# Performance work log

Hardware: AMD Instinct MI355X
Metric: run time of the kernel (lower is better)

## Reference

```python
import jax, jax.numpy as jnp
import numpy as np

N, E, G = 50000, 800000, 16
H, C = 4, 64  # heads, per-head channels
NEG_SLOPE = 0.2

def gat_conv(x, src, dst, W, att_s, att_d, bias, heads, out_c, concat):
    # x: [N, Fin]; W: [Fin, heads*out_c]; att_s/att_d: [heads, out_c]
    h = (x @ W).reshape(N, heads, out_c)
    a_s = (h * att_s).sum(-1)              # [N, heads]
    a_d = (h * att_d).sum(-1)
    e = a_s[src] + a_d[dst]                # [E, heads]
    e = jnp.where(e >= 0, e, NEG_SLOPE * e)  # leaky_relu
    m = jax.ops.segment_max(e, dst, num_segments=N)
    ex = jnp.exp(e - m[dst])
    den = jax.ops.segment_sum(ex, dst, num_segments=N)
    alpha = ex / (den[dst] + 1e-16)        # segment softmax over incoming edges
    msg = h[src] * alpha[:, :, None]       # [E, heads, out_c]
    out = jax.ops.segment_sum(msg, dst, num_segments=N)
    out = out.reshape(N, heads * out_c) if concat else out.mean(axis=1)
    return out + bias

def setup_inputs() -> dict:
    key = jax.random.key(0)
    ks = jax.random.split(key, 30)
    def g(k, shape, scale=0.05):
        return (jax.random.normal(k, shape, dtype=jnp.float32) * scale)
    inp = {}
    inp['x'] = jax.random.normal(ks[0], (N, 32), dtype=jnp.float32)
    inp['edge_index'] = jax.random.randint(ks[1], (2, E), 0, N, dtype=jnp.int32)
    inp['batch'] = jnp.sort(jax.random.randint(ks[2], (N,), 0, G, dtype=jnp.int32))
    inp['global_features'] = jax.random.normal(ks[3], (G, 4), dtype=jnp.float32)
    # node encoder
    inp['W_enc'] = g(ks[4], (32, C)); inp['b_enc'] = g(ks[5], (C,))
    # conv1: 64 -> 4x64 concat
    inp['W1'] = g(ks[6], (C, H * C)); inp['as1'] = g(ks[7], (H, C)); inp['ad1'] = g(ks[8], (H, C)); inp['b1'] = g(ks[9], (H * C,))
    # conv2: 256 -> 4x64 concat
    inp['W2'] = g(ks[10], (H * C, H * C)); inp['as2'] = g(ks[11], (H, C)); inp['ad2'] = g(ks[12], (H, C)); inp['b2'] = g(ks[13], (H * C,))
    # conv3: 256 -> 1x64 no concat
    inp['W3'] = g(ks[14], (H * C, C)); inp['as3'] = g(ks[15], (1, C)); inp['ad3'] = g(ks[16], (1, C)); inp['b3'] = g(ks[17], (C,))
    # global processor
    inp['Wg'] = g(ks[18], (4, C)); inp['bg'] = g(ks[19], (C,))
    # decoder
    inp['Wd1'] = g(ks[20], (2 * C, C)); inp['bd1'] = g(ks[21], (C,))
    inp['gamma'] = jnp.ones((C,), jnp.float32); inp['beta'] = jnp.zeros((C,), jnp.float32)
    inp['Wd2'] = g(ks[22], (C, 256)); inp['bd2'] = g(ks[23], (256,))
    return inp

def reference(x, edge_index, batch, global_features, W_enc, b_enc,
              W1, as1, ad1, b1, W2, as2, ad2, b2, W3, as3, ad3, b3,
              Wg, bg, Wd1, bd1, gamma, beta, Wd2, bd2):
    # add self-loops (PyG GATConv default)
    loops = jnp.arange(N, dtype=edge_index.dtype)
    src = jnp.concatenate([edge_index[0], loops])
    dst = jnp.concatenate([edge_index[1], loops])
    h = x @ W_enc + b_enc
    h = gat_conv(h, src, dst, W1, as1, ad1, b1, H, C, True)
    h = jax.nn.elu(h)  # dropout is identity in eval
    h = gat_conv(h, src, dst, W2, as2, ad2, b2, H, C, True)
    h = jax.nn.elu(h)
    h = gat_conv(h, src, dst, W3, as3, ad3, b3, 1, C, False)
    # global mean pool per graph
    sums = jax.ops.segment_sum(h, batch, num_segments=G)
    cnts = jax.ops.segment_sum(jnp.ones((N, 1), h.dtype), batch, num_segments=G)
    pooled = sums / jnp.maximum(cnts, 1.0)
    genc = jax.nn.relu(global_features @ Wg + bg)
    z = jnp.concatenate([pooled, genc], axis=1)
    z = z @ Wd1 + bd1
    z = z * gamma + beta  # BatchNorm1d in eval mode (running stats 0/1)
    z = jax.nn.relu(z)
    out = z @ Wd2 + bd2
    return jax.nn.softmax(out, axis=1)
```

## Files before the change

### kernel.cpp

```cpp
#include <hip/hip_runtime.h>
#include <math.h>

#define NEG_SLOPE 0.2f
#define LOG2E 1.4426950408889634f

typedef __attribute__((ext_vector_type(8))) short short8;
typedef __attribute__((ext_vector_type(4))) float f32x4;
typedef __attribute__((ext_vector_type(2))) float f32x2;

#if __has_builtin(__builtin_amdgcn_cvt_pk_f32_fp8) && __has_builtin(__builtin_amdgcn_cvt_pk_fp8_f32)
#define FP8_HW 1
#else
#define FP8_HW 0
#endif

__device__ inline float b2f_lo(unsigned int u) {
    union { unsigned int i; float f; } x; x.i = u << 16; return x.f;
}
__device__ inline float b2f_hi(unsigned int u) {
    union { unsigned int i; float f; } x; x.i = u & 0xFFFF0000u; return x.f;
}
__device__ inline unsigned short f2b(float f) {
    union { float f; unsigned int i; } u; u.f = f;
    unsigned int r = u.i + 0x7FFF + ((u.i >> 16) & 1);
    return (unsigned short)(r >> 16);
}

__device__ inline float fp8_decode1(unsigned int b) {
    unsigned int e = (b >> 3) & 15, m = b & 7;
    union { unsigned int i; float f; } u;
    if (e == 0) u.f = (float)m * 0.001953125f;
    else u.i = ((e + 120) << 23) | (m << 20);
    if (b & 0x80) u.f = -u.f;
    return u.f;
}
__device__ inline void fp8x4_to_f32(unsigned int g, float& v0, float& v1,
                                    float& v2, float& v3) {
#if FP8_HW
    f32x2 lo = __builtin_amdgcn_cvt_pk_f32_fp8((int)g, false);
    f32x2 hi = __builtin_amdgcn_cvt_pk_f32_fp8((int)g, true);
    v0 = lo[0]; v1 = lo[1]; v2 = hi[0]; v3 = hi[1];
#else
    v0 = fp8_decode1(g & 255);         v1 = fp8_decode1((g >> 8) & 255);
    v2 = fp8_decode1((g >> 16) & 255); v3 = fp8_decode1((g >> 24) & 255);
#endif
}
__device__ inline void fp8x2_to_f32(unsigned int g2, float& v0, float& v1) {
#if FP8_HW
    f32x2 lo = __builtin_amdgcn_cvt_pk_f32_fp8((int)(g2 & 0xFFFF), false);
    v0 = lo[0]; v1 = lo[1];
#else
    v0 = fp8_decode1(g2 & 255);
    v1 = fp8_decode1((g2 >> 8) & 255);
#endif
}
__device__ inline unsigned char f32_to_fp8(float f) {
#if FP8_HW
    return (unsigned char)(__builtin_amdgcn_cvt_pk_fp8_f32(f, f, 0, false) & 0xFF);
#else
    union { float f; unsigned int i; } u; u.f = f;
    unsigned int s = (u.i >> 24) & 0x80;
    float a = fabsf(f);
    if (a < 0.015625f) {
        int m = (int)rintf(a * 512.0f);
        if (m > 7) return (unsigned char)(s | 0x08);
        return (unsigned char)(s | m);
    }
    if (a >= 448.0f) return (unsigned char)(s | 0x7E);
    int e = (int)((u.i >> 23) & 0xFF) - 127;
    union { unsigned int i; float f; } sc; sc.i = (unsigned int)(127 + 3 - e) << 23;
    int q = (int)rintf(a * sc.f);
    if (q >= 16) { q = 8; e += 1; }
    return (unsigned char)(s | ((unsigned int)(e + 7) << 3) | (unsigned int)(q - 8));
#endif
}

__global__ void prep_kernel(const float* __restrict__ W_enc, const float* __restrict__ b_enc,
                            const float* __restrict__ W1, const float* __restrict__ W2,
                            const float* __restrict__ W3, const float* __restrict__ as1,
                            const float* __restrict__ ad1, const float* __restrict__ b1,
                            const float* __restrict__ as3, const float* __restrict__ ad3,
                            unsigned short* __restrict__ Wc1t, float* __restrict__ bc1,
                            unsigned short* __restrict__ Wt2, unsigned short* __restrict__ Wt3,
                            float* __restrict__ u1s, float* __restrict__ u1d,
                            float* __restrict__ u3s, float* __restrict__ u3d,
                            int* __restrict__ counts, float* __restrict__ pooledP,
                            float* __restrict__ cntP, int N, int G, int zc) {
    const int b = blockIdx.x;
    const int t = threadIdx.x;
    if (b < 32) {
        int i = b * 256 + t;
        int h = i >> 11, rem = i & 2047, o = rem >> 5, j = rem & 31;
        float s = 0.0f;
        for (int k = 0; k < 64; k++)
            s += W_enc[j * 64 + k] * W1[k * 256 + h * 64 + o];
        Wc1t[i] = f2b(s);
    } else if (b == 32) {
        float s = b1[t];
        for (int k = 0; k < 64; k++) s += b_enc[k] * W1[k * 256 + t];
        bc1[t] = s;
    } else if (b == 33) {
        int k = t >> 2, h = t & 3;
        float s = 0.0f, d = 0.0f;
        for (int c = 0; c < 64; c++) {
            float w = W1[k * 256 + h * 64 + c];
            s += w * as1[h * 64 + c];
            d += w * ad1[h * 64 + c];
        }
        u1s[k * 4 + h] = s;
        u1d[k * 4 + h] = d;
    } else if (b == 34) {
        float s = 0.0f, d = 0.0f;
        for (int o = 0; o < 64; o++) {
            float w = W3[t * 64 + o];
            s += w * as3[o];
            d += w * ad3[o];
        }
        u3s[t] = s; u3d[t] = d;
    } else if (b < 35 + 256) {
        int i = (b - 35) * 256 + t;
        int k = i >> 8, m = i & 255;
        Wt2[(size_t)m * 256 + k] = f2b(W2[i]);
    } else if (b < 35 + 256 + 64) {
        int i = (b - 291) * 256 + t;
        int k = i >> 6, m = i & 63;
        Wt3[(size_t)m * 256 + k] = f2b(W3[i]);
    } else if (b < 355 + zc) {
        int i = (b - 355) * 256 + t;
        if (i < N) counts[i] = 0;
    } else {
        int i = (b - 355 - zc) * 256 + t;
        if (i < 64 * G * 64) pooledP[i] = 0.0f;
        if (i < 64 * G) cntP[i] = 0.0f;
    }
}

__global__ __launch_bounds__(256) void score_x(
        const float* __restrict__ x, const float* __restrict__ W_enc,
        const float* __restrict__ b_enc,
        const float* __restrict__ u1s, const float* __restrict__ u1d,
        unsigned char* __restrict__ x8, float* __restrict__ a_s,
        float* __restrict__ a_d, int N) {
    __shared__ float sUs[32][4], sUd[32][4], sC[8];
    __shared__ float sX[32][33];
    const int t = threadIdx.x;
    if (t < 128) {
        int j = t >> 2, h = t & 3;
        float s = 0.0f, d = 0.0f;
        for (int k = 0; k < 64; k++) {
            float w = W_enc[j * 64 + k];
            s += w * u1s[k * 4 + h];
            d += w * u1d[k * 4 + h];
        }
        sUs[j][h] = s; sUd[j][h] = d;
    } else if (t < 136) {
        int hh = t - 128;
        const float* u = (hh < 4) ? u1s : u1d;
        int h = hh & 3;
        float c = 0.0f;
        for (int k = 0; k < 64; k++) c += b_enc[k] * u[k * 4 + h];
        sC[hh] = c;
    }
    const int n0 = blockIdx.x * 32;
    const int row = t >> 3, col = (t & 7) << 2;
    float4 xv = {0, 0, 0, 0};
    if (n0 + row < N) xv = *(const float4*)&x[(size_t)(n0 + row) * 32 + col];
    sX[row][col + 0] = xv.x; sX[row][col + 1] = xv.y;
    sX[row][col + 2] = xv.z; sX[row][col + 3] = xv.w;
    __syncthreads();
    const int ni = t >> 3, oi = t & 7, h = oi & 3;
    const bool isS = oi < 4;
    float acc = sC[oi];
    #pragma unroll 8
    for (int j = 0; j < 32; j++) acc += sX[ni][j] * (isS ? sUs[j][h] : sUd[j][h]);
    if (n0 + ni < N) {
        float* out = isS ? a_s : a_d;
        out[(size_t)(n0 + ni) * 4 + h] = acc * LOG2E;
    }
    if (n0 + row < N) {
        unsigned int o = (unsigned int)f32_to_fp8(xv.x)
                       | ((unsigned int)f32_to_fp8(xv.y) << 8)
                       | ((unsigned int)f32_to_fp8(xv.z) << 16)
                       | ((unsigned int)f32_to_fp8(xv.w) << 24);
        *(unsigned int*)&x8[(size_t)(n0 + row) * 32 + col] = o;
    }
}

__global__ __launch_bounds__(256) void gemm_c12(
        const unsigned short* __restrict__ aggX,
        const unsigned short* __restrict__ Wc1t,
        const float* __restrict__ bc1,
        const unsigned short* __restrict__ Wt2,
        const float* __restrict__ att_s,
        const float* __restrict__ att_d,
        float* __restrict__ a_s, float* __restrict__ a_d,
        unsigned char* __restrict__ C8,
        int Nrows) {
    __shared__ unsigned short sH[64][264];
    __shared__ unsigned short sB[256][40];
    __shared__ float sSD[64][4][2];
    const int tid = threadIdx.x;
    const int wave = tid >> 6;
    const int lane = tid & 63;
    const int quad = lane >> 4;
    const int l16 = lane & 15;
    const int row0 = blockIdx.x * 64;
    const int sr = tid >> 2;
    const int sk = (tid & 3) << 3;

    #pragma unroll
    for (int h = 0; h < 4; h++) {
        __syncthreads();
        {
            int r = row0 + sr;
            uint4 z = {0,0,0,0};
            *(uint4*)&sB[sr][sk] = (r < Nrows)
                ? *(const uint4*)&aggX[(size_t)r * 128 + h * 32 + sk] : z;
            *(uint4*)&sB[64 + sr][sk] = *(const uint4*)&Wc1t[(size_t)(h * 64 + sr) * 32 + sk];
        }
        __syncthreads();
        short8 bf = *(const short8*)&sB[64 + wave * 16 + l16][quad * 8];
        const int col = h * 64 + wave * 16 + l16;
        const float bb = bc1[col];
        #pragma unroll
        for (int i = 0; i < 4; i++) {
            short8 af = *(const short8*)&sB[i * 16 + l16][quad * 8];
            f32x4 acc = __builtin_amdgcn_mfma_f32_16x16x32_bf16(af, bf, (f32x4){0,0,0,0}, 0, 0, 0);
            #pragma unroll
            for (int r = 0; r < 4; r++) {
                float v = acc[r] + bb;
                v = (v > 0.0f) ? v : expm1f(v);
                sH[i * 16 + quad * 4 + r][col] = f2b(v);
            }
        }
    }

    f32x4 acc2[4][4];
    #pragma unroll
    for (int i = 0; i < 4; i++)
        #pragma unroll
        for (int j = 0; j < 4; j++) acc2[i][j] = (f32x4){0,0,0,0};

    for (int kt = 0; kt < 256; kt += 32) {
        __syncthreads();
        #pragma unroll
        for (int i = 0; i < 4; i++) {
            int c = sr + i * 64;
            *(uint4*)&sB[c][sk] = *(const uint4*)&Wt2[(size_t)c * 256 + kt + sk];
        }
        __syncthreads();
        short8 bf2[4];
        #pragma unroll
        for (int j = 0; j < 4; j++)
            bf2[j] = *(const short8*)&sB[wave * 64 + j * 16 + l16][quad * 8];
        #pragma unroll
        for (int i = 0; i < 4; i++) {
            short8 af = *(const short8*)&sH[i * 16 + l16][kt + quad * 8];
            #pragma unroll
            for (int j = 0; j < 4; j++)
                acc2[i][j] = __builtin_amdgcn_mfma_f32_16x16x32_bf16(af, bf2[j], acc2[i][j], 0, 0, 0);
        }
    }

    {
        for (int t = tid; t < 512; t += 256) ((float*)sSD)[t] = 0.0f;
        __syncthreads();
        float avs[4], avd[4];
        #pragma unroll
        for (int j = 0; j < 4; j++) {
            int c = wave * 64 + j * 16 + l16;
            avs[j] = att_s[c];
            avd[j] = att_d[c];
        }
        #pragma unroll
        for (int i = 0; i < 4; i++) {
            float ps[4] = {0,0,0,0}, pd[4] = {0,0,0,0};
            #pragma unroll
            for (int j = 0; j < 4; j++)
                #pragma unroll
                for (int r = 0; r < 4; r++) {
                    ps[r] += acc2[i][j][r] * avs[j];
                    pd[r] += acc2[i][j][r] * avd[j];
                }
            #pragma unroll
            for (int off = 1; off < 16; off <<= 1)
                #pragma unroll
                for (int r = 0; r < 4; r++) {
                    ps[r] += __shfl_xor(ps[r], off);
                    pd[r] += __shfl_xor(pd[r], off);
                }
            if (l16 == 0) {
                #pragma unroll
                for (int r = 0; r < 4; r++) {
                    atomicAdd(&sSD[i * 16 + quad * 4 + r][wave][0], ps[r]);
                    atomicAdd(&sSD[i * 16 + quad * 4 + r][wave][1], pd[r]);
                }
            }
        }
        __syncthreads();
        {
            int row = tid & 63, hb = tid >> 6;
            int r = row0 + row;
            if (r < Nrows) {
                a_s[r * 4 + hb] = sSD[row][hb][0] * LOG2E;
                a_d[r * 4 + hb] = sSD[row][hb][1] * LOG2E;
            }
        }
    }
    #pragma unroll
    for (int i = 0; i < 4; i++) {
        #pragma unroll
        for (int j = 0; j < 4; j++) {
            int col = wave * 64 + j * 16 + l16;
            #pragma unroll
            for (int r = 0; r < 4; r++) {
                int row = row0 + i * 16 + quad * 4 + r;
                if (row < Nrows) C8[(size_t)row * 256 + col] = f32_to_fp8(acc2[i][j][r]);
            }
        }
    }
}

__global__ __launch_bounds__(256) void gemm_c3(const unsigned short* __restrict__ A16,
                                               const unsigned short* __restrict__ Bt16,
                                               unsigned char* __restrict__ C8,
                                               int Nrows) {
    __shared__ unsigned short sA[64][40];
    __shared__ unsigned short sB[64][40];
    const int tid = threadIdx.x;
    const int wave = tid >> 6;
    const int lane = tid & 63;
    const int quad = lane >> 4;
    const int l16 = lane & 15;
    const int row0 = blockIdx.x * 64;
    const int sr = tid >> 2;
    const int sk = (tid & 3) << 3;

    f32x4 acc[4];
    #pragma unroll
    for (int i = 0; i < 4; i++) acc[i] = (f32x4){0,0,0,0};

    for (int kt = 0; kt < 256; kt += 32) {
        __syncthreads();
        {
            int r = row0 + sr;
            uint4 z = {0,0,0,0};
            *(uint4*)&sA[sr][sk] = (r < Nrows) ? *(const uint4*)&A16[(size_t)r * 256 + kt + sk] : z;
            *(uint4*)&sB[sr][sk] = *(const uint4*)&Bt16[(size_t)sr * 256 + kt + sk];
        }
        __syncthreads();
        short8 bf = *(const short8*)&sB[wave * 16 + l16][quad * 8];
        #pragma unroll
        for (int i = 0; i < 4; i++) {
            short8 af = *(const short8*)&sA[i * 16 + l16][quad * 8];
            acc[i] = __builtin_amdgcn_mfma_f32_16x16x32_bf16(af, bf, acc[i], 0, 0, 0);
        }
    }
    const int col = wave * 16 + l16;
    #pragma unroll
    for (int i = 0; i < 4; i++) {
        #pragma unroll
        for (int r = 0; r < 4; r++) {
            int row = row0 + i * 16 + quad * 4 + r;
            if (row < Nrows) C8[(size_t)row * 64 + col] = f32_to_fp8(acc[i][r]);
        }
    }
}

__global__ void edge_hist_kernel(const int* __restrict__ ei, int* __restrict__ counts,
                                 int E, int Et) {
    int e = blockIdx.x * 256 + threadIdx.x;
    if (e >= Et) return;
    int d = (e < E) ? ei[E + e] : e - E;
    atomicAdd(&counts[d], 1);
}

__global__ __launch_bounds__(1024) void scan_blocks(int* __restrict__ counts,
                                                    int* __restrict__ blockSums, int N) {
    __shared__ int wsum[16];
    const int tid = threadIdx.x;
    const int lane = tid & 63;
    const int wave = tid >> 6;
    int i = blockIdx.x * 1024 + tid;
    int v = (i < N) ? counts[i] : 0;
    int s = v;
    #pragma unroll
    for (int off = 1; off < 64; off <<= 1) {
        int t = __shfl_up(s, off);
        if (lane >= off) s += t;
    }
    if (lane == 63) wsum[wave] = s;
    __syncthreads();
    if (wave == 0 && lane < 16) {
        int ws = wsum[lane];
        #pragma unroll
        for (int off = 1; off < 16; off <<= 1) {
            int t = __shfl_up(ws, off);
            if (lane >= off) ws += t;
        }
        wsum[lane] = ws;
    }
    __syncthreads();
    int waveOff = (wave > 0) ? wsum[wave - 1] : 0;
    int incl = s + waveOff;
    if (i < N) counts[i] = incl - v;
    if (tid == 1023) blockSums[blockIdx.x] = incl;
}

__global__ void scan_add2(const int* __restrict__ excl, const int* __restrict__ blockSums,
                          int nb, int* __restrict__ offsets, int* __restrict__ cursor,
                          int N, int Et) {
    __shared__ int sbs[64];
    if (threadIdx.x < 64) {
        int lane = threadIdx.x;
        int v = (lane < nb) ? blockSums[lane] : 0;
        int s = v;
        #pragma unroll
        for (int off = 1; off < 64; off <<= 1) {
            int t = __shfl_up(s, off);
            if (lane >= off) s += t;
        }
        sbs[lane] = s - v;
    }
    __syncthreads();
    int i = blockIdx.x * 256 + threadIdx.x;
    if (i < N) {
        int o = excl[i] + sbs[i >> 10];
        offsets[i] = o;
        cursor[i] = o;
    }
    if (i == N) offsets[N] = Et;
}

__global__ void edge_sort_kernel(const int* __restrict__ ei, int* __restrict__ cursor,
                                 int* __restrict__ srcS, int E, int Et) {
    int e = blockIdx.x * 256 + threadIdx.x;
    if (e >= Et) return;
    int s, d;
    if (e < E) { s = ei[e]; d = ei[E + e]; } else { s = d = e - E; }
    int pos = atomicAdd(&cursor[d], 1);
    srcS[pos] = s;
}

__global__ __launch_bounds__(256) void gat_agg_x32(
        const int* __restrict__ offsets, const int* __restrict__ srcS,
        const float4* __restrict__ a_s4, const float4* __restrict__ a_d4,
        const unsigned char* __restrict__ x8,
        unsigned short* __restrict__ aggX,
        int N) {
    __shared__ float4 wlds[4][64];
    __shared__ int slds[4][64];
    const int wid = threadIdx.x >> 6;
    const int n = blockIdx.x * 4 + wid;
    if (n >= N) return;
    const int lane = threadIdx.x & 63;
    const int q = lane >> 4;
    const int l16 = lane & 15;
    const int start = offsets[n], end = offsets[n + 1];
    const float4 ad = a_d4[n];
    float2 acc0 = {0,0}, acc1 = {0,0}, acc2 = {0,0}, acc3 = {0,0};
    float4 den = {0,0,0,0};
    const int loff = l16 << 1;

    for (int e0 = start; e0 < end; e0 += 64) {
        const int cnt = min(64, end - e0);
        if (lane < cnt) {
            int sB = srcS[e0 + lane];
            slds[wid][lane] = sB;
            const float4 as = a_s4[sB];
            float x0 = as.x + ad.x; x0 = fmaxf(x0, NEG_SLOPE * x0);
            float x1 = as.y + ad.y; x1 = fmaxf(x1, NEG_SLOPE * x1);
            float x2 = as.z + ad.z; x2 = fmaxf(x2, NEG_SLOPE * x2);
            float x3 = as.w + ad.w; x3 = fmaxf(x3, NEG_SLOPE * x3);
            wlds[wid][lane] = (float4){exp2f(x0), exp2f(x1), exp2f(x2), exp2f(x3)};
        }
        int j = q;
        for (; j + 12 < cnt; j += 16) {
            int ss[4]; float4 ww[4]; unsigned int gg[4];
            #pragma unroll
            for (int u = 0; u < 4; u++) {
                ss[u] = slds[wid][j + 4 * u];
                ww[u] = wlds[wid][j + 4 * u];
            }
            #pragma unroll
            for (int u = 0; u < 4; u++)
                gg[u] = *(const unsigned short*)&x8[((size_t)ss[u] << 5) + loff];
            #pragma unroll
            for (int u = 0; u < 4; u++) {
                float vl, vh;
                fp8x2_to_f32(gg[u], vl, vh);
                acc0.x += ww[u].x * vl; acc0.y += ww[u].x * vh;
                acc1.x += ww[u].y * vl; acc1.y += ww[u].y * vh;
                acc2.x += ww[u].z * vl; acc2.y += ww[u].z * vh;
                acc3.x += ww[u].w * vl; acc3.y += ww[u].w * vh;
                den.x += ww[u].x; den.y += ww[u].y; den.z += ww[u].z; den.w += ww[u].w;
            }
        }
        for (; j + 4 < cnt; j += 8) {
            const int s0 = slds[wid][j], s1 = slds[wid][j + 4];
            const float4 w0 = wlds[wid][j], w1 = wlds[wid][j + 4];
            const unsigned int g0 = *(const unsigned short*)&x8[((size_t)s0 << 5) + loff];
            const unsigned int g1 = *(const unsigned short*)&x8[((size_t)s1 << 5) + loff];
            float vl0, vh0, vl1, vh1;
            fp8x2_to_f32(g0, vl0, vh0);
            fp8x2_to_f32(g1, vl1, vh1);
            acc0.x += w0.x * vl0 + w1.x * vl1; acc0.y += w0.x * vh0 + w1.x * vh1;
            acc1.x += w0.y * vl0 + w1.y * vl1; acc1.y += w0.y * vh0 + w1.y * vh1;
            acc2.x += w0.z * vl0 + w1.z * vl1; acc2.y += w0.z * vh0 + w1.z * vh1;
            acc3.x += w0.w * vl0 + w1.w * vl1; acc3.y += w0.w * vh0 + w1.w * vh1;
            den.x += w0.x + w1.x; den.y += w0.y + w1.y;
            den.z += w0.z + w1.z; den.w += w0.w + w1.w;
        }
        for (; j < cnt; j += 4) {
            const int s = slds[wid][j];
            const float4 w = wlds[wid][j];
            const unsigned int g = *(const unsigned short*)&x8[((size_t)s << 5) + loff];
            float vl, vh;
            fp8x2_to_f32(g, vl, vh);
            acc0.x += w.x * vl; acc0.y += w.x * vh;
            acc1.x += w.y * vl; acc1.y += w.y * vh;
            acc2.x += w.z * vl; acc2.y += w.z * vh;
            acc3.x += w.w * vl; acc3.y += w.w * vh;
            den.x += w.x; den.y += w.y; den.z += w.z; den.w += w.w;
        }
    }
    #pragma unroll
    for (int off = 16; off < 64; off <<= 1) {
        acc0.x += __shfl_xor(acc0.x, off); acc0.y += __shfl_xor(acc0.y, off);
        acc1.x += __shfl_xor(acc1.x, off); acc1.y += __shfl_xor(acc1.y, off);
        acc2.x += __shfl_xor(acc2.x, off); acc2.y += __shfl_xor(acc2.y, off);
        acc3.x += __shfl_xor(acc3.x, off); acc3.y += __shfl_xor(acc3.y, off);
        den.x += __shfl_xor(den.x, off); den.y += __shfl_xor(den.y, off);
        den.z += __shfl_xor(den.z, off); den.w += __shfl_xor(den.w, off);
    }
    if (q == 0) {
        const float i0 = 1.0f / (den.x + 1e-16f);
        const float i1 = 1.0f / (den.y + 1e-16f);
        const float i2 = 1.0f / (den.z + 1e-16f);
        const float i3 = 1.0f / (den.w + 1e-16f);
        unsigned int o0 = (unsigned int)f2b(acc0.x * i0) | ((unsigned int)f2b(acc0.y * i0) << 16);
        unsigned int o1 = (unsigned int)f2b(acc1.x * i1) | ((unsigned int)f2b(acc1.y * i1) << 16);
        unsigned int o2 = (unsigned int)f2b(acc2.x * i2) | ((unsigned int)f2b(acc2.y * i2) << 16);
        unsigned int o3 = (unsigned int)f2b(acc3.x * i3) | ((unsigned int)f2b(acc3.y * i3) << 16);
        *(unsigned int*)&aggX[((size_t)n << 7) + 0 * 32 + loff] = o0;
        *(unsigned int*)&aggX[((size_t)n << 7) + 1 * 32 + loff] = o1;
        *(unsigned int*)&aggX[((size_t)n << 7) + 2 * 32 + loff] = o2;
        *(unsigned int*)&aggX[((size_t)n << 7) + 3 * 32 + loff] = o3;
    }
}

__global__ __launch_bounds__(256) void gat_fused4(
        const int* __restrict__ offsets, const int* __restrict__ srcS,
        const float4* __restrict__ a_s4, const float4* __restrict__ a_d4,
        const unsigned char* __restrict__ h8, const float* __restrict__ bias,
        const float* __restrict__ u3s, const float* __restrict__ u3d,
        float* __restrict__ a_s3, float* __restrict__ a_d3,
        unsigned short* __restrict__ out16, int N) {
    __shared__ float wlds[4][64][4];
    __shared__ int slds[4][64];
    const int wid = threadIdx.x >> 6;
    const int n = blockIdx.x * 4 + wid;
    if (n >= N) return;
    const int lane = threadIdx.x & 63;
    const int quad = lane >> 4;
    const int start = offsets[n], end = offsets[n + 1];
    const float4 ad = a_d4[n];
    float4 acc = {0, 0, 0, 0};
    float den = 0.0f;
    const int loff = lane << 2;

    for (int e0 = start; e0 < end; e0 += 64) {
        const int cnt = min(64, end - e0);
        if (lane < cnt) {
            int sB = srcS[e0 + lane];
            slds[wid][lane] = sB;
            const float4 as = a_s4[sB];
            float x0 = as.x + ad.x; x0 = fmaxf(x0, NEG_SLOPE * x0);
            float x1 = as.y + ad.y; x1 = fmaxf(x1, NEG_SLOPE * x1);
            float x2 = as.z + ad.z; x2 = fmaxf(x2, NEG_SLOPE * x2);
            float x3 = as.w + ad.w; x3 = fmaxf(x3, NEG_SLOPE * x3);
            wlds[wid][lane][0] = exp2f(x0);
            wlds[wid][lane][1] = exp2f(x1);
            wlds[wid][lane][2] = exp2f(x2);
            wlds[wid][lane][3] = exp2f(x3);
        }
        int j = 0;
        for (; j + 4 <= cnt; j += 4) {
            const int s0 = __builtin_amdgcn_readfirstlane(slds[wid][j + 0]);
            const int s1 = __builtin_amdgcn_readfirstlane(slds[wid][j + 1]);
            const int s2 = __builtin_amdgcn_readfirstlane(slds[wid][j + 2]);
            const int s3 = __builtin_amdgcn_readfirstlane(slds[wid][j + 3]);
            const float w0 = wlds[wid][j + 0][quad];
            const float w1 = wlds[wid][j + 1][quad];
            const float w2 = wlds[wid][j + 2][quad];
            const float w3 = wlds[wid][j + 3][quad];
            const unsigned int g0 = *(const unsigned int*)&h8[((size_t)s0 << 8) + loff];
            const unsigned int g1 = *(const unsigned int*)&h8[((size_t)s1 << 8) + loff];
            const unsigned int g2 = *(const unsigned int*)&h8[((size_t)s2 << 8) + loff];
            const unsigned int g3 = *(const unsigned int*)&h8[((size_t)s3 << 8) + loff];
            float v0, v1, v2, v3;
            fp8x4_to_f32(g0, v0, v1, v2, v3);
            acc.x += w0 * v0; acc.y += w0 * v1; acc.z += w0 * v2; acc.w += w0 * v3;
            fp8x4_to_f32(g1, v0, v1, v2, v3);
            acc.x += w1 * v0; acc.y += w1 * v1; acc.z += w1 * v2; acc.w += w1 * v3;
            fp8x4_to_f32(g2, v0, v1, v2, v3);
            acc.x += w2 * v0; acc.y += w2 * v1; acc.z += w2 * v2; acc.w += w2 * v3;
            fp8x4_to_f32(g3, v0, v1, v2, v3);
            acc.x += w3 * v0; acc.y += w3 * v1; acc.z += w3 * v2; acc.w += w3 * v3;
            den += (w0 + w1) + (w2 + w3);
        }
        for (; j < cnt; j++) {
            const int s = __builtin_amdgcn_readfirstlane(slds[wid][j]);
            const float w = wlds[wid][j][quad];
            const unsigned int g = *(const unsigned int*)&h8[((size_t)s << 8) + loff];
            float v0, v1, v2, v3;
            fp8x4_to_f32(g, v0, v1, v2, v3);
            acc.x += w * v0; acc.y += w * v1; acc.z += w * v2; acc.w += w * v3;
            den += w;
        }
    }

    const float inv = 1.0f / (den + 1e-16f);
    const float4 bb = *(const float4*)&bias[loff];
    float v0 = acc.x * inv + bb.x; v0 = (v0 > 0.0f) ? v0 : expm1f(v0);
    float v1 = acc.y * inv + bb.y; v1 = (v1 > 0.0f) ? v1 : expm1f(v1);
    float v2 = acc.z * inv + bb.z; v2 = (v2 > 0.0f) ? v2 : expm1f(v2);
    float v3 = acc.w * inv + bb.w; v3 = (v3 > 0.0f) ? v3 : expm1f(v3);
    {
        const float4 us = *(const float4*)&u3s[loff];
        const float4 ud = *(const float4*)&u3d[loff];
        float ps = v0 * us.x + v1 * us.y + v2 * us.z + v3 * us.w;
        float pd = v0 * ud.x + v1 * ud.y + v2 * ud.z + v3 * ud.w;
        #pragma unroll
        for (int off = 1; off < 64; off <<= 1) {
            ps += __shfl_xor(ps, off);
            pd += __shfl_xor(pd, off);
        }
        if (lane == 0) {
            a_s3[n] = ps * LOG2E;
            a_d3[n] = pd * LOG2E;
        }
    }
    uint2 o;
    o.x = (unsigned int)f2b(v0) | ((unsigned int)f2b(v1) << 16);
    o.y = (unsigned int)f2b(v2) | ((unsigned int)f2b(v3) << 16);
    *(uint2*)&out16[(size_t)n * 256 + loff] = o;
}

__global__ __launch_bounds__(256) void gat_fused1(
        const int* __restrict__ offsets, const int* __restrict__ srcS,
        const float* __restrict__ a_s, const float* __restrict__ a_d,
        const unsigned char* __restrict__ h8, const float* __restrict__ bias,
        const int* __restrict__ batch,
        float* __restrict__ pooledP, float* __restrict__ cntP, int N, int G) {
    __shared__ float wlds[4][64];
    __shared__ int slds[4][64];
    __shared__ float2 sOut[4][32];
    __shared__ int sG[4];
    const int wid = threadIdx.x >> 6;
    const int n = blockIdx.x * 4 + wid;
    const bool valid = n < N;
    const int lane = threadIdx.x & 63;
    const int half = lane >> 5;
    const int l32 = lane & 31;
    const int start = valid ? offsets[n] : 0;
    const int end   = valid ? offsets[n + 1] : 0;
    const float ad  = valid ? a_d[n] : 0.0f;
    float accx = 0.0f, accy = 0.0f, den = 0.0f;
    const int loff = l32 << 1;

    for (int e0 = start; e0 < end; e0 += 64) {
        const int cnt_ = min(64, end - e0);
        if (lane < cnt_) {
            int sB = srcS[e0 + lane];
            slds[wid][lane] = sB;
            float ev = a_s[sB] + ad;
            ev = fmaxf(ev, NEG_SLOPE * ev);
            wlds[wid][lane] = exp2f(ev);
        }
        int j = half;
        for (; j + 8 <= cnt_ + half; j += 8) {
            const int s0 = slds[wid][j + 0];
            const int s1 = slds[wid][j + 2];
            const int s2 = slds[wid][j + 4];
            const int s3 = slds[wid][j + 6];
            const float w0 = wlds[wid][j + 0];
            const float w1 = wlds[wid][j + 2];
            const float w2 = wlds[wid][j + 4];
            const float w3 = wlds[wid][j + 6];
            const unsigned int g0 = *(const unsigned short*)&h8[((size_t)s0 << 6) + loff];
            const unsigned int g1 = *(const unsigned short*)&h8[((size_t)s1 << 6) + loff];
            const unsigned int g2 = *(const unsigned short*)&h8[((size_t)s2 << 6) + loff];
            const unsigned int g3 = *(const unsigned short*)&h8[((size_t)s3 << 6) + loff];
            float vl, vh;
            fp8x2_to_f32(g0, vl, vh); accx += w0 * vl; accy += w0 * vh;
            fp8x2_to_f32(g1, vl, vh); accx += w1 * vl; accy += w1 * vh;
            fp8x2_to_f32(g2, vl, vh); accx += w2 * vl; accy += w2 * vh;
            fp8x2_to_f32(g3, vl, vh); accx += w3 * vl; accy += w3 * vh;
            den += (w0 + w1) + (w2 + w3);
        }
        for (; j < cnt_; j += 2) {
            const int s = slds[wid][j];
            const float w = wlds[wid][j];
            const unsigned int g = *(const unsigned short*)&h8[((size_t)s << 6) + loff];
            float vl, vh;
            fp8x2_to_f32(g, vl, vh);
            accx += w * vl;
            accy += w * vh;
            den += w;
        }
    }
    accx += __shfl_xor(accx, 32);
    accy += __shfl_xor(accy, 32);
    den  += __shfl_xor(den, 32);
    if (half == 0) {
        if (valid) {
            const float inv = 1.0f / (den + 1e-16f);
            sOut[wid][l32] = (float2){accx * inv + bias[loff], accy * inv + bias[loff + 1]};
        } else {
            sOut[wid][l32] = (float2){0.0f, 0.0f};
        }
        if (l32 == 0) sG[wid] = valid ? batch[n] : -1;
    }
    __syncthreads();
    const int p = blockIdx.x & 63;
    if (wid == 0 && half == 0) {
        const int g0 = sG[0], g1 = sG[1], g2 = sG[2], g3 = sG[3];
        if (g0 >= 0 && g1 == g0 && g2 == g0 && g3 == g0) {
            const float2 s0 = sOut[0][l32], s1 = sOut[1][l32];
            const float2 s2 = sOut[2][l32], s3 = sOut[3][l32];
            float* base = pooledP + ((size_t)p * G + g0) * 64;
            atomicAdd(&base[loff],     (s0.x + s1.x) + (s2.x + s3.x));
            atomicAdd(&base[loff + 1], (s0.y + s1.y) + (s2.y + s3.y));
            if (l32 == 0) atomicAdd(&cntP[p * G + g0], 4.0f);
        } else {
            #pragma unroll
            for (int w = 0; w < 4; w++) {
                const int g = sG[w];
                if (g >= 0) {
                    const float2 s = sOut[w][l32];
                    float* base = pooledP + ((size_t)p * G + g) * 64;
                    atomicAdd(&base[loff], s.x);
                    atomicAdd(&base[loff + 1], s.y);
                    if (l32 == 0) atomicAdd(&cntP[p * G + g], 1.0f);
                }
            }
        }
    }
}

__global__ __launch_bounds__(256) void final_kernel(
        const float* __restrict__ pooledP, const float* __restrict__ cntP,
        const float* __restrict__ gf, const float* __restrict__ Wg,
        const float* __restrict__ bg, const float* __restrict__ Wd1,
        const float* __restrict__ bd1, const float* __restrict__ gamma,
        const float* __restrict__ beta, const float* __restrict__ Wd2,
        const float* __restrict__ bd2, float* __restrict__ out, int G) {
    const int g = blockIdx.x;
    const int tid = threadIdx.x;
    const int lane = tid & 63;
    const int wave = tid >> 6;
    __shared__ float sPart[4][64];
    __shared__ float sCntTot;
    __shared__ float spg[128];
    __shared__ float sz[64];
    __shared__ float wred[8];

    {
        const int c = lane;
        const int pg = wave;
        float a = 0.0f;
        #pragma unroll
        for (int p = 0; p < 16; p++)
            a += pooledP[((size_t)(pg * 16 + p) * G + g) * 64 + c];
        sPart[pg][c] = a;
        if (pg == 1) {
            float cv = cntP[c * G + g];
            #pragma unroll
            for (int off = 32; off > 0; off >>= 1) cv += __shfl_xor(cv, off);
            if (c == 0) sCntTot = cv;
        }
    }
    __syncthreads();
    if (tid < 64) {
        spg[tid] = (sPart[0][tid] + sPart[1][tid] + sPart[2][tid] + sPart[3][tid])
                   / fmaxf(sCntTot, 1.0f);
    } else if (tid < 128) {
        int c = tid - 64;
        float v = bg[c];
        #pragma unroll
        for (int k = 0; k < 4; k++) v += gf[g * 4 + k] * Wg[k * 64 + c];
        spg[64 + c] = fmaxf(v, 0.0f);
    }
    __syncthreads();
    if (tid < 64) {
        float v = bd1[tid];
        #pragma unroll 8
        for (int k = 0; k < 128; k++) v += spg[k] * Wd1[k * 64 + tid];
        v = v * gamma[tid] + beta[tid];
        sz[tid] = fmaxf(v, 0.0f);
    }
    __syncthreads();
    float v = bd2[tid];
    #pragma unroll 8
    for (int k = 0; k < 64; k++) v += sz[k] * Wd2[k * 256 + tid];
    float m = v;
    #pragma unroll
    for (int off = 32; off > 0; off >>= 1) m = fmaxf(m, __shfl_xor(m, off));
    if (lane == 0) wred[wave] = m;
    __syncthreads();
    float M = fmaxf(fmaxf(wred[0], wred[1]), fmaxf(wred[2], wred[3]));
    float e = expf(v - M);
    float s = e;
    #pragma unroll
    for (int off = 32; off > 0; off >>= 1) s += __shfl_xor(s, off);
    if (lane == 0) wred[4 + wave] = s;
    __syncthreads();
    float S = (wred[4] + wred[5]) + (wred[6] + wred[7]);
    out[g * 256 + tid] = e / S;
}

extern "C" void kernel_launch(void* const* d_in, const int* in_sizes, int n_in,
                              void* d_out, int out_size, void* d_ws, size_t ws_size,
                              hipStream_t stream) {
    const float* x     = (const float*)d_in[0];
    const int*   ei    = (const int*)  d_in[1];
    const int*   batch = (const int*)  d_in[2];
    const float* gf    = (const float*)d_in[3];
    const float* W_enc = (const float*)d_in[4];
    const float* b_enc = (const float*)d_in[5];
    const float* W1  = (const float*)d_in[6];
    const float* as1 = (const float*)d_in[7];
    const float* ad1 = (const float*)d_in[8];
    const float* b1  = (const float*)d_in[9];
    const float* W2  = (const float*)d_in[10];
    const float* as2 = (const float*)d_in[11];
    const float* ad2 = (const float*)d_in[12];
    const float* b2  = (const float*)d_in[13];
    const float* W3  = (const float*)d_in[14];
    const float* as3 = (const float*)d_in[15];
    const float* ad3 = (const float*)d_in[16];
    const float* b3  = (const float*)d_in[17];
    const float* Wg  = (const float*)d_in[18];
    const float* bg  = (const float*)d_in[19];
    const float* Wd1 = (const float*)d_in[20];
    const float* bd1 = (const float*)d_in[21];
    const float* gm  = (const float*)d_in[22];
    const float* bt  = (const float*)d_in[23];
    const float* Wd2 = (const float*)d_in[24];
    const float* bd2 = (const float*)d_in[25];

    const int N  = in_sizes[2];
    const int E  = in_sizes[1] / 2;
    const int G  = in_sizes[3] / 4;
    const int Et = E + N;

    unsigned short* h16a = (unsigned short*)d_ws;
    unsigned short* h16b = h16a + (size_t)N * 256;
    unsigned short* h1_16 = h16b + (size_t)N * 256;
    unsigned short* x16  = h1_16 + (size_t)N * 64;
    unsigned short* Wc1t = x16 + (size_t)N * 32;
    unsigned short* Wt2  = Wc1t + 4 * 64 * 32;
    unsigned short* Wt3  = Wt2 + 256 * 256;
    float* bc1    = (float*)(Wt3 + 64 * 256);
    float* a_s    = bc1 + 256;
    float* a_d    = a_s + (size_t)N * 4;
    float* a_s3   = a_d + (size_t)N * 4;
    float* a_d3   = a_s3 + N;
    float* u1s    = a_d3 + N;
    float* u1d    = u1s + 256;
    float* u3s    = u1d + 256;
    float* u3d    = u3s + 256;
    float* pooledP = u3d + 256;
    float* cntP   = pooledP + (size_t)64 * G * 64;
    int*   offsets = (int*)(cntP + 64 * G);
    int*   srcS    = offsets + (N + 1);
    int*   counts  = srcS + Et;
    int*   cursor  = counts + N;
    int*   blockSums = cursor + N;

    unsigned char* h8a  = (unsigned char*)h16a;
    unsigned char* h1_8 = (unsigned char*)h1_16;
    unsigned char* x8   = (unsigned char*)x16;

    dim3 blk(256);
    auto cdiv = [](int a, int b) { return (a + b - 1) / b; };
    const int eBlocks = cdiv(Et, 256);
    const int rowBlocks = cdiv(N, 64);
    const int nScanBlocks = cdiv(N, 1024);
    const int zc = cdiv(N, 256);
    const int z2 = cdiv(64 * G * 64, 256);

    prep_kernel<<<355 + zc + z2, blk, 0, stream>>>(W_enc, b_enc, W1, W2, W3, as1, ad1, b1,
                                                   as3, ad3, Wc1t, bc1, Wt2, Wt3,
                                                   u1s, u1d, u3s, u3d,
                                                   counts, pooledP, cntP, N, G, zc);
    edge_hist_kernel<<<eBlocks, blk, 0, stream>>>(ei, counts, E, Et);
    scan_blocks<<<nScanBlocks, 1024, 0, stream>>>(counts, blockSums, N);
    scan_add2<<<cdiv(N + 1, 256), blk, 0, stream>>>(counts, blockSums, nScanBlocks,
                                                    offsets, cursor, N, Et);
    edge_sort_kernel<<<eBlocks, blk, 0, stream>>>(ei, cursor, srcS, E, Et);

    score_x<<<cdiv(N, 32), blk, 0, stream>>>(x, W_enc, b_enc, u1s, u1d, x8, a_s, a_d, N);

    gat_agg_x32<<<cdiv(N, 4), blk, 0, stream>>>(offsets, srcS, (const float4*)a_s,
                                                (const float4*)a_d, x8, h16b, N);
    gemm_c12<<<rowBlocks, blk, 0, stream>>>(h16b, Wc1t, bc1, Wt2, as2, ad2,
                                            a_s, a_d, h8a, N);

    gat_fused4<<<cdiv(N, 4), blk, 0, stream>>>(offsets, srcS, (const float4*)a_s,
                                               (const float4*)a_d, h8a, b2,
                                               u3s, u3d, a_s3, a_d3, h16b, N);

    gemm_c3<<<rowBlocks, blk, 0, stream>>>(h16b, Wt3, h1_8, N);
    gat_fused1<<<cdiv(N, 4), blk, 0, stream>>>(offsets, srcS, a_s3, a_d3, h1_8, b3,
                                               batch, pooledP, cntP, N, G);

    final_kernel<<<G, blk, 0, stream>>>(pooledP, cntP, gf, Wg, bg, Wd1, bd1, gm, bt, Wd2, bd2,
                                        (float*)d_out, G);
}
```

Measured before the change: 378.8 us.

## Replace atomic CSR edge sort with two-level bucketed counting sort

The single-pass scatter that used global per-node atomic cursors is replaced by a two-level sort. Edges are first binned into buckets of 128 destination nodes, using block-local shared histograms and one global atomic per bucket per block. Each bucket is then sorted into CSR order by one block using shared-memory counters. The aim is to cut heavily contended global atomics and improve write locality when scattering the source indices. In exchange it adds an extra pass over an 8-byte-per-edge intermediate buffer and two more kernel launches. The edge order within each node still depends on atomic scheduling, so results remain nondeterministic.

```diff
diff --git a/kernel.cpp b/kernel.cpp
--- a/kernel.cpp
+++ b/kernel.cpp
@@ -3,6 +3,7 @@
 
 #define NEG_SLOPE 0.2f
 #define LOG2E 1.4426950408889634f
+#define BSH 7
 
 typedef __attribute__((ext_vector_type(8))) short short8;
 typedef __attribute__((ext_vector_type(4))) float f32x4;
@@ -85,7 +86,8 @@
                             float* __restrict__ u1s, float* __restrict__ u1d,
                             float* __restrict__ u3s, float* __restrict__ u3d,
                             int* __restrict__ counts, float* __restrict__ pooledP,
-                            float* __restrict__ cntP, int N, int G, int zc) {
+                            float* __restrict__ cntP, int* __restrict__ bucketCnt,
+                            int N, int G, int zc, int NB) {
     const int b = blockIdx.x;
     const int t = threadIdx.x;
     if (b < 32) {
@@ -132,6 +134,7 @@
         int i = (b - 355 - zc) * 256 + t;
         if (i < 64 * G * 64) pooledP[i] = 0.0f;
         if (i < 64 * G) cntP[i] = 0.0f;
+        if (i <= NB) bucketCnt[i] = 0;
     }
 }
 
@@ -367,12 +370,29 @@
     }
 }
 
-__global__ void edge_hist_kernel(const int* __restrict__ ei, int* __restrict__ counts,
-                                 int E, int Et) {
-    int e = blockIdx.x * 256 + threadIdx.x;
-    if (e >= Et) return;
-    int d = (e < E) ? ei[E + e] : e - E;
-    atomicAdd(&counts[d], 1);
+__global__ __launch_bounds__(256) void edge_hist_kernel(const int* __restrict__ ei,
+                                                        int* __restrict__ counts,
+                                                        int* __restrict__ bucketCnt,
+                                                        int E, int Et, int NB) {
+    __shared__ int lhist[1024];
+    const int tid = threadIdx.x;
+    for (int b = tid; b < NB; b += 256) lhist[b] = 0;
+    __syncthreads();
+    const int base = blockIdx.x * 4096;
+    #pragma unroll
+    for (int k = 0; k < 16; k++) {
+        int e = base + k * 256 + tid;
+        if (e < Et) {
+            int d = (e < E) ? ei[E + e] : e - E;
+            atomicAdd(&counts[d], 1);
+            atomicAdd(&lhist[d >> BSH], 1);
+        }
+    }
+    __syncthreads();
+    for (int b = tid; b < NB; b += 256) {
+        int h = lhist[b];
+        if (h > 0) atomicAdd(&bucketCnt[b], h);
+    }
 }
 
 __global__ __launch_bounds__(1024) void scan_blocks(int* __restrict__ counts,
@@ -408,8 +428,7 @@
 }
 
 __global__ void scan_add2(const int* __restrict__ excl, const int* __restrict__ blockSums,
-                          int nb, int* __restrict__ offsets, int* __restrict__ cursor,
-                          int N, int Et) {
+                          int nb, int* __restrict__ offsets, int N, int Et) {
     __shared__ int sbs[64];
     if (threadIdx.x < 64) {
         int lane = threadIdx.x;
@@ -424,22 +443,90 @@
     }
     __syncthreads();
     int i = blockIdx.x * 256 + threadIdx.x;
-    if (i < N) {
-        int o = excl[i] + sbs[i >> 10];
-        offsets[i] = o;
-        cursor[i] = o;
-    }
+    if (i < N) offsets[i] = excl[i] + sbs[i >> 10];
     if (i == N) offsets[N] = Et;
 }
 
-__global__ void edge_sort_kernel(const int* __restrict__ ei, int* __restrict__ cursor,
-                                 int* __restrict__ srcS, int E, int Et) {
-    int e = blockIdx.x * 256 + threadIdx.x;
-    if (e >= Et) return;
-    int s, d;
-    if (e < E) { s = ei[e]; d = ei[E + e]; } else { s = d = e - E; }
-    int pos = atomicAdd(&cursor[d], 1);
-    srcS[pos] = s;
+__global__ __launch_bounds__(1024) void bucket_scan(const int* __restrict__ bucketCnt,
+                                                    int* __restrict__ bucketOff,
+                                                    int* __restrict__ bucketCur,
+                                                    int NB, int Et) {
+    __shared__ int s[1024];
+    const int tid = threadIdx.x;
+    int v = (tid < NB) ? bucketCnt[tid] : 0;
+    s[tid] = v;
+    __syncthreads();
+    #pragma unroll
+    for (int off = 1; off < 1024; off <<= 1) {
+        int t = (tid >= off) ? s[tid - off] : 0;
+        __syncthreads();
+        s[tid] += t;
+        __syncthreads();
+    }
+    if (tid < NB) {
+        int ex = s[tid] - v;
+        bucketOff[tid] = ex;
+        bucketCur[tid] = ex;
+    }
+    if (tid == 0) bucketOff[NB] = Et;
+}
+
+__global__ __launch_bounds__(256) void bucket_scatter(const int* __restrict__ ei,
+                                                      int* __restrict__ bucketCur,
+                                                      uint2* __restrict__ bucketBuf,
+                                                      int E, int Et, int NB) {
+    __shared__ int lhist[1024];
+    __shared__ int lbase[1024];
+    const int tid = threadIdx.x;
+    for (int b = tid; b < NB; b += 256) lhist[b] = 0;
+    __syncthreads();
+    const int base = blockIdx.x * 4096;
+    int sv[16], dv[16];
+    #pragma unroll
+    for (int k = 0; k < 16; k++) {
+        int e = base + k * 256 + tid;
+        if (e < Et) {
+            int ss, dd;
+            if (e < E) { ss = ei[e]; dd = ei[E + e]; } else { ss = dd = e - E; }
+            sv[k] = ss; dv[k] = dd;
+            atomicAdd(&lhist[dd >> BSH], 1);
+        } else dv[k] = -1;
+    }
+    __syncthreads();
+    for (int b = tid; b < NB; b += 256) {
+        int h = lhist[b];
+        lbase[b] = (h > 0) ? atomicAdd(&bucketCur[b], h) : 0;
+    }
+    __syncthreads();
+    for (int b = tid; b < NB; b += 256) lhist[b] = 0;
+    __syncthreads();
+    #pragma unroll
+    for (int k = 0; k < 16; k++) {
+        if (dv[k] >= 0) {
+            int b = dv[k] >> BSH;
+            int r = atomicAdd(&lhist[b], 1);
+            bucketBuf[lbase[b] + r] = (uint2){(unsigned int)sv[k], (unsigned int)dv[k]};
+        }
+    }
+}
+
+__global__ __launch_bounds__(256) void bucket_sort(const uint2* __restrict__ bucketBuf,
+                                                   const int* __restrict__ bucketOff,
+                                                   const int* __restrict__ offsets,
+                                                   int* __restrict__ srcS) {
+    __shared__ int cnt[128];
+    const int tid = threadIdx.x;
+    const int b = blockIdx.x;
+    if (tid < 128) cnt[tid] = 0;
+    __syncthreads();
+    const int node0 = b << BSH;
+    const int s0 = bucketOff[b], s1 = bucketOff[b + 1];
+    for (int i = s0 + tid; i < s1; i += 256) {
+        uint2 e = bucketBuf[i];
+        int dl = (int)e.y - node0;
+        int r = atomicAdd(&cnt[dl], 1);
+        srcS[offsets[e.y] + r] = (int)e.x;
+    }
 }
 
 __global__ __launch_bounds__(256) void gat_agg_x32(
@@ -854,6 +941,7 @@
     const int E  = in_sizes[1] / 2;
     const int G  = in_sizes[3] / 4;
     const int Et = E + N;
+    const int NB = (N + 127) >> 7;
 
     unsigned short* h16a = (unsigned short*)d_ws;
     unsigned short* h16b = h16a + (size_t)N * 256;
@@ -876,8 +964,11 @@
     int*   offsets = (int*)(cntP + 64 * G);
     int*   srcS    = offsets + (N + 1);
     int*   counts  = srcS + Et;
-    int*   cursor  = counts + N;
-    int*   blockSums = cursor + N;
+    int*   blockSums = counts + N;
+    int*   bucketCnt = blockSums + ((N + 1023) / 1024);
+    int*   bucketOff = bucketCnt + (NB + 1);
+    int*   bucketCur = bucketOff + (NB + 1);
+    uint2* bucketBuf = (uint2*)(((size_t)(bucketCur + NB) + 7) & ~(size_t)7);
 
     unsigned char* h8a  = (unsigned char*)h16a;
     unsigned char* h1_8 = (unsigned char*)h1_16;
@@ -885,7 +976,7 @@
 
     dim3 blk(256);
     auto cdiv = [](int a, int b) { return (a + b - 1) / b; };
-    const int eBlocks = cdiv(Et, 256);
+    const int ebBlocks = cdiv(Et, 4096);
     const int rowBlocks = cdiv(N, 64);
     const int nScanBlocks = cdiv(N, 1024);
     const int zc = cdiv(N, 256);
@@ -894,12 +985,15 @@
     prep_kernel<<<355 + zc + z2, blk, 0, stream>>>(W_enc, b_enc, W1, W2, W3, as1, ad1, b1,
                                                    as3, ad3, Wc1t, bc1, Wt2, Wt3,
                                                    u1s, u1d, u3s, u3d,
-                                                   counts, pooledP, cntP, N, G, zc);
-    edge_hist_kernel<<<eBlocks, blk, 0, stream>>>(ei, counts, E, Et);
+                                                   counts, pooledP, cntP, bucketCnt,
+                                                   N, G, zc, NB);
+    edge_hist_kernel<<<ebBlocks, blk, 0, stream>>>(ei, counts, bucketCnt, E, Et, NB);
     scan_blocks<<<nScanBlocks, 1024, 0, stream>>>(counts, blockSums, N);
     scan_add2<<<cdiv(N + 1, 256), blk, 0, stream>>>(counts, blockSums, nScanBlocks,
-                                                    offsets, cursor, N, Et);
-    edge_sort_kernel<<<eBlocks, blk, 0, stream>>>(ei, cursor, srcS, E, Et);
+                                                    offsets, N, Et);
+    bucket_scan<<<1, 1024, 0, stream>>>(bucketCnt, bucketOff, bucketCur, NB, Et);
+    bucket_scatter<<<ebBlocks, blk, 0, stream>>>(ei, bucketCur, bucketBuf, E, Et, NB);
+    bucket_sort<<<NB, blk, 0, stream>>>(bucketBuf, bucketOff, offsets, srcS);
 
     score_x<<<cdiv(N, 32), blk, 0, stream>>>(x, W_enc, b_enc, u1s, u1d, x8, a_s, a_d, N);
 
```

Result: faster. 354.1 us (-6.5%).
